# Performance work log

Measured on AMD Instinct MI355X. Metric: run time of the kernel, lower is better.

## Reference

```python
import jax, jax.numpy as jnp
import numpy as np

MESH_SIZE = 0.01
TEMP = 0.001
T = 4096
HID = (16, 16, 16)


def _triangle_mesh():
    g = np.arange(-1.0, 1.0 + 1e-9, MESH_SIZE, dtype=np.float32)  # 201 pts
    A, B = np.meshgrid(g, g, indexing='ij')  # alpha rows, beta cols
    mask = A >= B                             # Preisach triangle alpha >= beta
    return A[mask].astype(np.float32), B[mask].astype(np.float32)  # [N], [N]


def _constrain(v, lo, hi):
    return lo + (hi - lo) * jax.nn.sigmoid(v)


def setup_inputs() -> dict:
    key = jax.random.key(0)
    ks = jax.random.split(key, 12)
    alpha_np, beta_np = _triangle_mesh()
    N = alpha_np.shape[0]  # 20301

    def xavier(k, fan_in, fan_out):
        b = np.sqrt(6.0 / (fan_in + fan_out)).astype(np.float32)
        return jax.random.uniform(k, (fan_in, fan_out), jnp.float32, -b, b)

    dims = (2,) + HID + (1,)
    params = {}
    for i in range(4):
        params[f'w{i+1}'] = xavier(ks[i], dims[i], dims[i + 1])
        params[f'b{i+1}'] = jnp.zeros((dims[i + 1],), jnp.float32)

    bound = np.sqrt(6.0 / (1 + N)).astype(np.float32)  # xavier_uniform on (1,N)
    init_state_raw = jax.random.uniform(ks[10], (N,), jnp.float32, -bound, bound)

    return dict(
        x=jax.random.normal(ks[11], (T,), jnp.float32),
        alpha_raw=jnp.asarray(alpha_np),
        beta_raw=jnp.asarray(beta_np),
        init_state_raw=init_state_raw,
        m_scale_raw=jnp.asarray(1.0, jnp.float32),
        m_offset_raw=jnp.asarray(1.0, jnp.float32),
        h_scale_raw=jnp.asarray(1.0, jnp.float32),
        **params,
    )


def _get_states(x, alpha, beta, s0, temp):
    # Soft Preisach relay: switch up where u>alpha, down where u<beta, else hold.
    def step(s, u):
        up = jax.nn.sigmoid((u - alpha) / temp)
        dn = jax.nn.sigmoid((beta - u) / temp)
        s_new = up - dn + (1.0 - up) * (1.0 - dn) * s
        return s_new, s_new
    _, states = jax.lax.scan(step, s0, x)
    return states  # [T, N]


def reference(x, alpha_raw, beta_raw, init_state_raw,
              w1, b1, w2, b2, w3, b3, w4, b4,
              m_scale_raw, m_offset_raw, h_scale_raw):
    alpha = alpha_raw  # ConstrainedParameter with no bounds -> identity
    beta = beta_raw
    s0 = jnp.tanh(init_state_raw)  # BinaryParameter (soft binary)

    states = _get_states(x, alpha, beta, s0, TEMP)  # [T, N]

    mesh = jnp.stack([alpha, beta], axis=1)  # [N, 2]
    h = jax.nn.relu(mesh @ w1 + b1)
    h = jax.nn.relu(h @ w2 + b2)
    h = jax.nn.relu(h @ w3 + b3)
    density = jax.nn.sigmoid(h @ w4 + b4)  # [N, 1]
    density = density.T  # [1, N]

    m = jnp.sum(density * states, axis=-1) / jnp.sum(density, axis=-1)  # [T]

    m_scale = _constrain(m_scale_raw, 0.0, 10.0)
    m_offset = _constrain(m_offset_raw, -10.0, 10.0)
    h_scale = _constrain(h_scale_raw, 0.0, 10.0)

    out = m_scale * m + m_offset + h_scale * x  # [T]
    return out, density, states
```

## Files before the change

kernel.cpp:

```cpp
#include <hip/hip_runtime.h>
#include <math.h>

#define NM 20301
#define TT 4096
#define NC 64
#define CH 64
#define NBLK 80
#define SBLK 20
#define NPROW (SBLK * 4)
#define NROWS (NPROW + 80)
#define TPH 16
#define NPH (CH / TPH)
#define LOG2E_K 1442.69504f
#define WNEAR 26.0f

__device__ __forceinline__ void relay_step(float ka, float kb, float ku,
                                           float& aa, float& bb) {
    float z1 = fminf(ka - ku, 63.f);
    float z2 = fminf(ku - kb, 63.f);
    float e1 = __builtin_amdgcn_exp2f(z1);
    float e2 = __builtin_amdgcn_exp2f(z2);
    float p1 = 1.f + e1, p2 = 1.f + e2;
    float r  = __builtin_amdgcn_rcpf(p1 * p2);
    aa = (e2 - e1) * r;
    bb = (e1 * e2) * r;
}

__device__ __forceinline__ float wave_reduce_sum(float w) {
    #pragma unroll
    for (int off = 32; off > 0; off >>= 1)
        w += __shfl_down(w, off, 64);
    return w;
}

__global__ __launch_bounds__(256) void density_kernel(
    const float* __restrict__ alpha, const float* __restrict__ beta,
    const float* __restrict__ w1, const float* __restrict__ b1,
    const float* __restrict__ w2, const float* __restrict__ b2,
    const float* __restrict__ w3, const float* __restrict__ b3,
    const float* __restrict__ w4, const float* __restrict__ b4,
    float* __restrict__ density_out, float* __restrict__ densum_parts)
{
    int n = blockIdx.x * 256 + threadIdx.x;
    bool valid = n < NM;
    int nn = valid ? n : NM - 1;
    float a = alpha[nn], b = beta[nn];

    float h1[16], h2[16], h3[16];
    #pragma unroll
    for (int j = 0; j < 16; j++) {
        float v = fmaf(a, w1[j], fmaf(b, w1[16 + j], b1[j]));
        h1[j] = fmaxf(v, 0.f);
    }
    #pragma unroll
    for (int j = 0; j < 16; j++) {
        float v = b2[j];
        #pragma unroll
        for (int k = 0; k < 16; k++) v = fmaf(h1[k], w2[k * 16 + j], v);
        h2[j] = fmaxf(v, 0.f);
    }
    #pragma unroll
    for (int j = 0; j < 16; j++) {
        float v = b3[j];
        #pragma unroll
        for (int k = 0; k < 16; k++) v = fmaf(h2[k], w3[k * 16 + j], v);
        h3[j] = fmaxf(v, 0.f);
    }
    float v = b4[0];
    #pragma unroll
    for (int k = 0; k < 16; k++) v = fmaf(h3[k], w4[k], v);
    float d = 1.f / (1.f + __expf(-v));

    if (valid) density_out[n] = d;
    float wsum = wave_reduce_sum(valid ? d : 0.f);
    __shared__ float ws_[4];
    if ((threadIdx.x & 63) == 0) ws_[threadIdx.x >> 6] = wsum;
    __syncthreads();
    if (threadIdx.x == 0)
        densum_parts[blockIdx.x] = ws_[0] + ws_[1] + ws_[2] + ws_[3];
}

__global__ __launch_bounds__(256) void states_spec_kernel(
    const float* __restrict__ x, const float* __restrict__ alpha,
    const float* __restrict__ beta, const float* __restrict__ density,
    float* __restrict__ states, float* __restrict__ partials,
    float* __restrict__ Acomp, float* __restrict__ Bcomp)
{
    __shared__ float xs[CH];
    __shared__ float tile[4 * 64 * (TPH + 1)];

    int tid = threadIdx.x;
    int c = blockIdx.y;
    if (tid < CH) xs[tid] = x[c * CH + tid] * LOG2E_K;

    int n0 = blockIdx.x * 1024 + tid;
    float A[4], B[4], d[4], ka[4], kb[4];
    bool v[4];
    #pragma unroll
    for (int q = 0; q < 4; q++) {
        int n = n0 + q * 256;
        v[q] = n < NM;
        int nn = v[q] ? n : NM - 1;
        ka[q] = alpha[nn] * LOG2E_K;
        kb[q] = beta[nn] * LOG2E_K;
        d[q]  = v[q] ? density[n] : 0.f;
        A[q] = 0.f; B[q] = 1.f;
    }
    __syncthreads();

    int wv = tid >> 6, ln = tid & 63;
    int tl = ln & 15, h = ln >> 4;
    float* wtile = &tile[wv * 64 * (TPH + 1)];
    float* tslot = &wtile[ln * (TPH + 1)];
    float* rp    = states + (size_t)c * CH * NM + n0;
    size_t prow  = (size_t)(blockIdx.x * 4 + wv) * TT + c * CH;

    #pragma unroll 1
    for (int p = 0; p < NPH; p++) {
        float xr[TPH];
        #pragma unroll
        for (int j = 0; j < TPH; j++) xr[j] = xs[p * TPH + j];
        #pragma unroll
        for (int j = 0; j < TPH; j++) {
            float u = xr[j];
            float w1_[4], w2_[4], nr[4];
            #pragma unroll
            for (int q = 0; q < 4; q++) {
                w1_[q] = ka[q] - u;
                w2_[q] = u - kb[q];
                nr[q]  = fminf(fabsf(w1_[q]), fabsf(w2_[q]));
            }
            float nmin = fminf(fminf(nr[0], nr[1]), fminf(nr[2], nr[3]));
            if (__any(nmin < WNEAR)) {
                #pragma unroll
                for (int q = 0; q < 4; q++) {
                    float aa, bb;
                    relay_step(ka[q], kb[q], u, aa, bb);
                    A[q] = fmaf(bb, A[q], aa);
                    B[q] *= bb;
                }
            } else {
                #pragma unroll
                for (int q = 0; q < 4; q++) {
                    bool su = w1_[q] < 0.f, sd = w2_[q] < 0.f;
                    A[q] = su ? 1.f : (sd ? -1.f : A[q]);
                    B[q] = (su || sd) ? 0.f : B[q];
                }
            }
            #pragma unroll
            for (int q = 0; q < 4; q++)
                if (v[q]) rp[q * 256] = A[q];
            rp += NM;
            tslot[j] = fmaf(d[0], A[0], fmaf(d[1], A[1],
                       fmaf(d[2], A[2], d[3] * A[3])));
        }
        asm volatile("s_waitcnt lgkmcnt(0)" ::: "memory");
        float acc = 0.f;
        #pragma unroll
        for (int k = 0; k < TPH; k++)
            acc += wtile[(h * 16 + k) * (TPH + 1) + tl];
        acc += __shfl_xor(acc, 16, 64);
        acc += __shfl_xor(acc, 32, 64);
        if (ln < TPH) partials[prow + p * TPH + ln] = acc;
        asm volatile("s_waitcnt lgkmcnt(0)" ::: "memory");
    }

    #pragma unroll
    for (int q = 0; q < 4; q++) {
        if (v[q]) {
            Acomp[(size_t)c * NM + n0 + q * 256] = A[q];
            Bcomp[(size_t)c * NM + n0 + q * 256] = B[q];
        }
    }
}

__global__ __launch_bounds__(256) void senter_kernel(
    const float* __restrict__ init_raw,
    const float* __restrict__ Acomp, const float* __restrict__ Bcomp,
    float* __restrict__ senter)
{
    int n = blockIdx.x * 256 + threadIdx.x;
    if (n >= NM) return;
    float s = tanhf(init_raw[n]);
    float a0[16], b0[16], a1[16], b1[16];
    #pragma unroll
    for (int k = 0; k < 16; k++) {
        a0[k] = Acomp[(size_t)k * NM + n];
        b0[k] = Bcomp[(size_t)k * NM + n];
    }
    #pragma unroll
    for (int qtr = 0; qtr < 4; qtr++) {
        if (qtr < 3) {
            #pragma unroll
            for (int k = 0; k < 16; k++) {
                if (qtr & 1) {
                    a0[k] = Acomp[(size_t)((qtr + 1) * 16 + k) * NM + n];
                    b0[k] = Bcomp[(size_t)((qtr + 1) * 16 + k) * NM + n];
                } else {
                    a1[k] = Acomp[(size_t)((qtr + 1) * 16 + k) * NM + n];
                    b1[k] = Bcomp[(size_t)((qtr + 1) * 16 + k) * NM + n];
                }
            }
        }
        #pragma unroll
        for (int k = 0; k < 16; k++) {
            senter[(size_t)(qtr * 16 + k) * NM + n] = s;
            if (qtr & 1) s = fmaf(b1[k], s, a1[k]);
            else         s = fmaf(b0[k], s, a0[k]);
        }
    }
}

__global__ __launch_bounds__(256) void patch_kernel(
    const float* __restrict__ x, const float* __restrict__ alpha,
    const float* __restrict__ beta, const float* __restrict__ density,
    const float* __restrict__ senter,
    float* __restrict__ states, float* __restrict__ partials)
{
    __shared__ float xsl[CH];
    int tid = threadIdx.x;
    int c = blockIdx.y, bx = blockIdx.x;
    if (tid < CH) xsl[tid] = x[c * CH + tid] * LOG2E_K;

    int n0 = bx * 1024 + tid;
    float ka[4], kb[4], d[4], se[4], ss[4], Bf[4];
    bool v[4];
    #pragma unroll
    for (int q = 0; q < 4; q++) {
        int n = n0 + q * 256;
        v[q] = n < NM;
        int nn = v[q] ? n : NM - 1;
        ka[q] = alpha[nn] * LOG2E_K;
        kb[q] = beta[nn] * LOG2E_K;
        d[q]  = v[q] ? density[n] : 0.f;
        se[q] = senter[(size_t)c * NM + nn];
        ss[q] = se[q];
        Bf[q] = 1.f;
    }
    __syncthreads();

    int wv = tid >> 6, ln = tid & 63;
    float myval = 0.f;
    float* rp = states + (size_t)c * CH * NM + n0;
    #pragma unroll 1
    for (int j = 0; j < CH; j++) {
        bool live = (Bf[0] != 0.f) | (Bf[1] != 0.f) |
                    (Bf[2] != 0.f) | (Bf[3] != 0.f);
        if (!__any(live)) break;
        float u = xsl[j];
        float contrib = 0.f;
        #pragma unroll
        for (int q = 0; q < 4; q++) {
            float aa, bb;
            relay_step(ka[q], kb[q], u, aa, bb);
            Bf[q] *= bb;
            ss[q] = fmaf(bb, ss[q], aa);
            if (Bf[q] != 0.f) {
                if (v[q]) rp[q * 256] = ss[q];
                contrib = fmaf(d[q] * Bf[q], se[q], contrib);
            }
        }
        rp += NM;
        #pragma unroll
        for (int off = 1; off < 64; off <<= 1)
            contrib += __shfl_xor(contrib, off, 64);
        if (ln == j) myval = contrib;
    }
    partials[(size_t)(NPROW + bx * 4 + wv) * TT + c * CH + ln] = myval;
}

__global__ __launch_bounds__(256) void finalize_kernel(
    const float* __restrict__ x, const float* __restrict__ partials,
    const float* __restrict__ densum_parts,
    const float* __restrict__ msr, const float* __restrict__ mor,
    const float* __restrict__ hsr, float* __restrict__ out)
{
    int t = blockIdx.x * 256 + threadIdx.x;
    if (t >= TT) return;
    float acc = 0.f;
    for (int r = 0; r < NROWS; r++)
        acc += partials[(size_t)r * TT + t];
    float dsum = 0.f;
    for (int bx = 0; bx < NBLK; bx++)
        dsum += densum_parts[bx];
    float sig_ms = 1.f / (1.f + __expf(-msr[0]));
    float sig_mo = 1.f / (1.f + __expf(-mor[0]));
    float sig_hs = 1.f / (1.f + __expf(-hsr[0]));
    float m_scale  = 10.f * sig_ms;
    float m_offset = fmaf(20.f, sig_mo, -10.f);
    float h_scale  = 10.f * sig_hs;
    float m = acc / dsum;
    out[t] = fmaf(m_scale, m, m_offset) + h_scale * x[t];
}

extern "C" void kernel_launch(void* const* d_in, const int* in_sizes, int n_in,
                              void* d_out, int out_size, void* d_ws, size_t ws_size,
                              hipStream_t stream)
{
    const float* x    = (const float*)d_in[0];
    const float* alpha= (const float*)d_in[1];
    const float* beta = (const float*)d_in[2];
    const float* init = (const float*)d_in[3];
    const float* msr  = (const float*)d_in[4];
    const float* mor  = (const float*)d_in[5];
    const float* hsr  = (const float*)d_in[6];
    const float* w1   = (const float*)d_in[7];
    const float* b1   = (const float*)d_in[8];
    const float* w2   = (const float*)d_in[9];
    const float* b2   = (const float*)d_in[10];
    const float* w3   = (const float*)d_in[11];
    const float* b3   = (const float*)d_in[12];
    const float* w4   = (const float*)d_in[13];
    const float* b4   = (const float*)d_in[14];

    float* out     = (float*)d_out;
    float* density = out + TT;
    float* states  = density + NM;

    float* densum_parts = (float*)d_ws;
    float* partials     = densum_parts + 128;
    float* Acomp        = partials + (size_t)NROWS * TT;
    float* Bcomp        = Acomp + (size_t)NC * NM;
    float* senter       = Bcomp + (size_t)NC * NM;

    density_kernel<<<dim3(NBLK), dim3(256), 0, stream>>>(
        alpha, beta, w1, b1, w2, b2, w3, b3, w4, b4,
        density, densum_parts);

    states_spec_kernel<<<dim3(SBLK, NC), dim3(256), 0, stream>>>(
        x, alpha, beta, density, states, partials, Acomp, Bcomp);

    senter_kernel<<<dim3(NBLK), dim3(256), 0, stream>>>(
        init, Acomp, Bcomp, senter);

    patch_kernel<<<dim3(SBLK, NC), dim3(256), 0, stream>>>(
        x, alpha, beta, density, senter, states, partials);

    finalize_kernel<<<dim3(TT / 256), dim3(256), 0, stream>>>(
        x, partials, densum_parts, msr, mor, hsr, out);
}
```

Before: 448.1 us.

## Halve time-chunk length, drop far-field fast path, use nontemporal state stores

Changes the time chunking from 64 chunks of 64 steps to 128 chunks of 32 steps, which doubles the chunk-level parallelism and shortens the sequential scan each block runs. The senter prefix kernel now loops over 8 batches of 16 chunks instead of 4. The saturated-relay fast path (the __any wave vote with the WNEAR threshold) is removed, so every step runs the full sigmoid relay. State writes now use nontemporal stores to limit cache pollution from the large states output. The costs are more exp/rcp work per step, a longer serial chain in senter, and more per-chunk overhead.

Result: slower. 493.9 us (+10.2%).

```diff
diff --git a/kernel.cpp b/kernel.cpp
--- a/kernel.cpp
+++ b/kernel.cpp
@@ -3,8 +3,8 @@
 
 #define NM 20301
 #define TT 4096
-#define NC 64
-#define CH 64
+#define NC 128
+#define CH 32
 #define NBLK 80
 #define SBLK 20
 #define NPROW (SBLK * 4)
@@ -12,7 +12,6 @@
 #define TPH 16
 #define NPH (CH / TPH)
 #define LOG2E_K 1442.69504f
-#define WNEAR 26.0f
 
 __device__ __forceinline__ void relay_step(float ka, float kb, float ku,
                                            float& aa, float& bb) {
@@ -123,33 +122,14 @@
         #pragma unroll
         for (int j = 0; j < TPH; j++) {
             float u = xr[j];
-            float w1_[4], w2_[4], nr[4];
             #pragma unroll
             for (int q = 0; q < 4; q++) {
-                w1_[q] = ka[q] - u;
-                w2_[q] = u - kb[q];
-                nr[q]  = fminf(fabsf(w1_[q]), fabsf(w2_[q]));
+                float aa, bb;
+                relay_step(ka[q], kb[q], u, aa, bb);
+                A[q] = fmaf(bb, A[q], aa);
+                B[q] *= bb;
+                if (v[q]) __builtin_nontemporal_store(A[q], rp + q * 256);
             }
-            float nmin = fminf(fminf(nr[0], nr[1]), fminf(nr[2], nr[3]));
-            if (__any(nmin < WNEAR)) {
-                #pragma unroll
-                for (int q = 0; q < 4; q++) {
-                    float aa, bb;
-                    relay_step(ka[q], kb[q], u, aa, bb);
-                    A[q] = fmaf(bb, A[q], aa);
-                    B[q] *= bb;
-                }
-            } else {
-                #pragma unroll
-                for (int q = 0; q < 4; q++) {
-                    bool su = w1_[q] < 0.f, sd = w2_[q] < 0.f;
-                    A[q] = su ? 1.f : (sd ? -1.f : A[q]);
-                    B[q] = (su || sd) ? 0.f : B[q];
-                }
-            }
-            #pragma unroll
-            for (int q = 0; q < 4; q++)
-                if (v[q]) rp[q * 256] = A[q];
             rp += NM;
             tslot[j] = fmaf(d[0], A[0], fmaf(d[1], A[1],
                        fmaf(d[2], A[2], d[3] * A[3])));
@@ -189,24 +169,20 @@
         b0[k] = Bcomp[(size_t)k * NM + n];
     }
     #pragma unroll
-    for (int qtr = 0; qtr < 4; qtr++) {
-        if (qtr < 3) {
+    for (int bt = 0; bt < 8; bt++) {
+        if (bt + 1 < 8) {
             #pragma unroll
             for (int k = 0; k < 16; k++) {
-                if (qtr & 1) {
-                    a0[k] = Acomp[(size_t)((qtr + 1) * 16 + k) * NM + n];
-                    b0[k] = Bcomp[(size_t)((qtr + 1) * 16 + k) * NM + n];
-                } else {
-                    a1[k] = Acomp[(size_t)((qtr + 1) * 16 + k) * NM + n];
-                    b1[k] = Bcomp[(size_t)((qtr + 1) * 16 + k) * NM + n];
-                }
+                size_t idx = (size_t)((bt + 1) * 16 + k) * NM + n;
+                if (bt & 1) { a0[k] = Acomp[idx]; b0[k] = Bcomp[idx]; }
+                else        { a1[k] = Acomp[idx]; b1[k] = Bcomp[idx]; }
             }
         }
         #pragma unroll
         for (int k = 0; k < 16; k++) {
-            senter[(size_t)(qtr * 16 + k) * NM + n] = s;
-            if (qtr & 1) s = fmaf(b1[k], s, a1[k]);
-            else         s = fmaf(b0[k], s, a0[k]);
+            senter[(size_t)(bt * 16 + k) * NM + n] = s;
+            if (bt & 1) s = fmaf(b1[k], s, a1[k]);
+            else        s = fmaf(b0[k], s, a0[k]);
         }
     }
 }
@@ -266,7 +242,8 @@
             contrib += __shfl_xor(contrib, off, 64);
         if (ln == j) myval = contrib;
     }
-    partials[(size_t)(NPROW + bx * 4 + wv) * TT + c * CH + ln] = myval;
+    if (ln < CH)
+        partials[(size_t)(NPROW + bx * 4 + wv) * TT + c * CH + ln] = myval;
 }
 
 __global__ __launch_bounds__(256) void finalize_kernel(
```
